# Performance work log

Measured on AMD Instinct MI355X. Metric: run time of the kernel, lower is better.

The kernel has to match this reference:

```python
import jax, jax.numpy as jnp
import numpy as np

B, S, HID = 1, 2048, 2048
NH, NKV = 32, 8
HD = HID // NH  # 64
WINDOW = 1024
ROPE_BASE = 500000.0


def setup_inputs() -> dict:
    key = jax.random.key(0)
    ks = jax.random.split(key, 5)
    sc = 0.02
    return {
        "hidden_states": jax.random.normal(ks[0], (B, S, HID), dtype=jnp.float32),
        "Wq": jax.random.normal(ks[1], (HID, NH * HD), dtype=jnp.float32) * sc,
        "Wk": jax.random.normal(ks[2], (HID, NKV * HD), dtype=jnp.float32) * sc,
        "Wv": jax.random.normal(ks[3], (HID, NKV * HD), dtype=jnp.float32) * sc,
        "Wo": jax.random.normal(ks[4], (NH * HD, HID), dtype=jnp.float32) * sc,
    }


def _rope_cos_sin(seq_len, dtype):
    inv_freq = 1.0 / (ROPE_BASE ** (jnp.arange(0, HD, 2, dtype=jnp.float32) / HD))
    pos = jnp.arange(seq_len, dtype=jnp.float32)
    freqs = pos[:, None] * inv_freq[None, :]          # [S, HD/2]
    emb = jnp.concatenate([freqs, freqs], axis=-1)    # [S, HD]
    return jnp.cos(emb).astype(dtype), jnp.sin(emb).astype(dtype)


def _rotate_half(x):
    x1, x2 = x[..., : HD // 2], x[..., HD // 2:]
    return jnp.concatenate([-x2, x1], axis=-1)


def reference(hidden_states, Wq, Wk, Wv, Wo):
    b, s, _ = hidden_states.shape
    q = (hidden_states @ Wq).reshape(b, s, NH, HD).transpose(0, 2, 1, 3)   # [B,NH,S,D]
    k = (hidden_states @ Wk).reshape(b, s, NKV, HD).transpose(0, 2, 1, 3)  # [B,NKV,S,D]
    v = (hidden_states @ Wv).reshape(b, s, NKV, HD).transpose(0, 2, 1, 3)

    cos, sin = _rope_cos_sin(s, hidden_states.dtype)  # [S, D]
    cos, sin = cos[None, None], sin[None, None]       # [1,1,S,D]
    q = q * cos + _rotate_half(q) * sin
    k = k * cos + _rotate_half(k) * sin

    n_rep = NH // NKV
    k = jnp.repeat(k, n_rep, axis=1)  # [B,NH,S,D]
    v = jnp.repeat(v, n_rep, axis=1)

    # sliding-window causal additive mask
    row = jnp.arange(s)[:, None]
    col = jnp.arange(s)[None, :]
    banned = (col > row) | (col < row - WINDOW + 1)
    mask = jnp.where(banned, jnp.float32(-jnp.inf), 0.0).astype(hidden_states.dtype)

    scale = 1.0 / np.sqrt(HD)
    scores = jnp.einsum("bhqd,bhkd->bhqk", q, k) * scale + mask
    attn = jax.nn.softmax(scores, axis=-1)
    out = jnp.einsum("bhqk,bhkd->bhqd", attn, v)          # [B,NH,S,D]
    out = out.transpose(0, 2, 1, 3).reshape(b, s, NH * HD)
    return out @ Wo
```

## Files before the change

kernel.cpp:

```cpp
#include <hip/hip_runtime.h>
#include <hip/hip_bf16.h>
#include <math.h>

#define S_LEN 2048
#define HID 2048
#define NH 32
#define NKV 8
#define HD 64
#define WINDOW 1024
#define QBLK 128
#define QKVN 3072

typedef __attribute__((ext_vector_type(8))) short bx8;
typedef __attribute__((ext_vector_type(4))) float fx4;
typedef __attribute__((ext_vector_type(8))) unsigned short us8;

#define GL_LDS16(gp, lp) \
    __builtin_amdgcn_global_load_lds((__attribute__((address_space(1))) const void*)(gp), \
                                     (__attribute__((address_space(3))) void*)(lp), 16, 0, 0)

__global__ __launch_bounds__(256) void prep_kernel(const float* __restrict__ hs,
                                                   const float* __restrict__ Wq,
                                                   const float* __restrict__ Wk,
                                                   const float* __restrict__ Wv,
                                                   const float* __restrict__ Wo,
                                                   float* __restrict__ cosT, float* __restrict__ sinT,
                                                   __hip_bfloat16* __restrict__ hsb,
                                                   __hip_bfloat16* __restrict__ WqkvT,
                                                   __hip_bfloat16* __restrict__ WoT) {
    __shared__ float tile[32][33];
    int b = blockIdx.x, t = threadIdx.x;
    if (b < 256) {
        int idx = b * 256 + t;
        int s = idx >> 5, f = idx & 31;
        double inv = exp(-2.0 * (double)f / 64.0 * log(500000.0));
        double ang = (double)s * inv;
        cosT[idx] = (float)cos(ang);
        sinT[idx] = (float)sin(ang);
        return;
    }
    b -= 256;
    if (b < 2048) {
        int i = (b * 256 + t) * 8;
        float4 a = *reinterpret_cast<const float4*>(&hs[i]);
        float4 c = *reinterpret_cast<const float4*>(&hs[i + 4]);
        __hip_bfloat16 o[8] __attribute__((aligned(16)));
        o[0] = __float2bfloat16(a.x); o[1] = __float2bfloat16(a.y);
        o[2] = __float2bfloat16(a.z); o[3] = __float2bfloat16(a.w);
        o[4] = __float2bfloat16(c.x); o[5] = __float2bfloat16(c.y);
        o[6] = __float2bfloat16(c.z); o[7] = __float2bfloat16(c.w);
        *reinterpret_cast<bx8*>(&hsb[i]) = *reinterpret_cast<bx8*>(o);
        return;
    }
    b -= 2048;
    const float* src; __hip_bfloat16* dst; int Nd, bx, by;
    if (b < 4096)      { src = Wq; dst = WqkvT;                        Nd = 2048; bx = b & 63; by = b >> 6; }
    else if (b < 5120) { b -= 4096; src = Wk; dst = WqkvT + (size_t)2048 * 2048; Nd = 512; bx = b & 15; by = b >> 4; }
    else if (b < 6144) { b -= 5120; src = Wv; dst = WqkvT + (size_t)2560 * 2048; Nd = 512; bx = b & 15; by = b >> 4; }
    else               { b -= 6144; src = Wo; dst = WoT;               Nd = 2048; bx = b & 63; by = b >> 6; }
    int n0 = bx * 32, k0 = by * 32, tx = t & 31, ty = t >> 5;
#pragma unroll
    for (int i = 0; i < 4; i++)
        tile[ty + 8 * i][tx] = src[(size_t)(k0 + ty + 8 * i) * Nd + n0 + tx];
    __syncthreads();
#pragma unroll
    for (int i = 0; i < 4; i++)
        dst[(size_t)(n0 + ty + 8 * i) * 2048 + k0 + tx] = __float2bfloat16(tile[tx][ty + 8 * i]);
}

__global__ __launch_bounds__(256) void ropev_kernel(__hip_bfloat16* __restrict__ QKV,
                                                    __hip_bfloat16* __restrict__ Vt,
                                                    const float* __restrict__ cosT,
                                                    const float* __restrict__ sinT) {
    __shared__ __hip_bfloat16 tile[32][33];
    int b = blockIdx.x, t = threadIdx.x;
    if (b < 10240) {
        int idx = b * 256 + t;
        int f = idx & 31;
        int head = (idx >> 5) % (NH + NKV);
        int s = idx / ((NH + NKV) * 32);
        float c  = cosT[(s << 5) + f];
        float sn = sinT[(s << 5) + f];
        __hip_bfloat16* p = (head < NH) ? (QKV + (size_t)s * QKVN + head * HD)
                                        : (QKV + (size_t)s * QKVN + 2048 + (head - NH) * HD);
        float x1 = __bfloat162float(p[f]), x2 = __bfloat162float(p[f + 32]);
        p[f]      = __float2bfloat16(x1 * c - x2 * sn);
        p[f + 32] = __float2bfloat16(x2 * c + x1 * sn);
        return;
    }
    b -= 10240;
    int s0 = (b & 63) * 32, d0 = (b >> 6) * 32;
    int tx = t & 31, ty = t >> 5;
#pragma unroll
    for (int i = 0; i < 4; i++)
        tile[ty + 8 * i][tx] = QKV[(size_t)(s0 + ty + 8 * i) * QKVN + 2560 + d0 + tx];
    __syncthreads();
#pragma unroll
    for (int i = 0; i < 4; i++)
        Vt[(size_t)(d0 + ty + 8 * i) * S_LEN + s0 + tx] = tile[tx][ty + 8 * i];
}

template <int OUTBF16>
__global__ __launch_bounds__(256) void gemm_pipe_kernel(const __hip_bfloat16* __restrict__ A,
                                                        const __hip_bfloat16* __restrict__ Bt,
                                                        void* __restrict__ Cp,
                                                        int M, int N, int K, int stripe) {
    __shared__ __hip_bfloat16 As[4][2048];
    __shared__ __hip_bfloat16 Bs[4][4096];

    const int bid = blockIdx.x;
    const int x = bid & 7, j = bid >> 3;
    const int bn = (x * stripe + j % stripe) * 128;
    const int bm = (j / stripe) * 64;

    const int t = threadIdx.x, w = t >> 6, l = t & 63;
    const int wr = (w >> 1) * 32, wc = (w & 1) * 64;
    const int lr = l & 15;
    const int rdslot = (((l >> 4) ^ ((lr >> 1) & 3))) * 8;
    const int srow = w * 16 + (l >> 2);
    const int scol = (((l & 3) ^ ((l >> 3) & 3))) * 8;
    const int ldsoff = w * 512;

    const __hip_bfloat16* ga0 = A + (size_t)(bm + srow) * K + scol;
    const __hip_bfloat16* gb0 = Bt + (size_t)(bn + srow) * K + scol;
    const size_t half = (size_t)64 * K;

    fx4 acc[2][4];
#pragma unroll
    for (int m = 0; m < 2; m++)
#pragma unroll
        for (int n = 0; n < 4; n++) acc[m][n] = (fx4){0.f, 0.f, 0.f, 0.f};

    const int T = K >> 5;

#define STAGE(kt, b)                                              \
    do {                                                          \
        const __hip_bfloat16* ga = ga0 + (kt) * 32;               \
        const __hip_bfloat16* gb = gb0 + (kt) * 32;               \
        GL_LDS16(ga,        &As[(b)][ldsoff]);                    \
        GL_LDS16(gb,        &Bs[(b)][ldsoff]);                    \
        GL_LDS16(gb + half, &Bs[(b)][2048 + ldsoff]);             \
    } while (0)

    STAGE(0, 0);
    STAGE(1, 1);
    STAGE(2, 2);

    for (int i = 0; i < T; i++) {
        const int r = i & 3;
        if (i + 2 < T)      asm volatile("s_waitcnt vmcnt(6)" ::: "memory");
        else if (i + 1 < T) asm volatile("s_waitcnt vmcnt(3)" ::: "memory");
        else                asm volatile("s_waitcnt vmcnt(0)" ::: "memory");
        __builtin_amdgcn_s_barrier();
        asm volatile("" ::: "memory");
        if (i + 3 < T) STAGE(i + 3, (i + 3) & 3);

        bx8 af[2], bf[4];
#pragma unroll
        for (int m = 0; m < 2; m++)
            af[m] = *reinterpret_cast<const bx8*>(&As[r][(wr + m * 16 + lr) * 32 + rdslot]);
#pragma unroll
        for (int n = 0; n < 4; n++)
            bf[n] = *reinterpret_cast<const bx8*>(&Bs[r][(wc + n * 16 + lr) * 32 + rdslot]);
#pragma unroll
        for (int m = 0; m < 2; m++)
#pragma unroll
            for (int n = 0; n < 4; n++)
                acc[m][n] = __builtin_amdgcn_mfma_f32_16x16x32_bf16(af[m], bf[n], acc[m][n], 0, 0, 0);
    }
#undef STAGE

    const int lq = (l >> 4) * 4;
#pragma unroll
    for (int m = 0; m < 2; m++)
#pragma unroll
        for (int n = 0; n < 4; n++)
#pragma unroll
            for (int r2 = 0; r2 < 4; r2++) {
                int row = bm + wr + m * 16 + lq + r2;
                int col = bn + wc + n * 16 + lr;
                float v = acc[m][n][r2];
                if (OUTBF16)
                    ((__hip_bfloat16*)Cp)[(size_t)row * N + col] = __float2bfloat16(v);
                else
                    ((float*)Cp)[(size_t)row * N + col] = v;
            }
}

__global__ __launch_bounds__(512, 4) void attn_kernel(const __hip_bfloat16* __restrict__ Q,
                                                      const __hip_bfloat16* __restrict__ Kg,
                                                      const __hip_bfloat16* __restrict__ Vtg,
                                                      __hip_bfloat16* __restrict__ Ab) {
    __shared__ __hip_bfloat16 Ks[2][4096];
    __shared__ __hip_bfloat16 Vs[2][4096];
    __shared__ __hip_bfloat16 Ps[QBLK * 64];

    const int bid = blockIdx.x;
    const int swz = (bid & 7) * 64 + (bid >> 3);
    const int h = swz >> 4, qi = swz & 15;
    const int qb = qi * QBLK;
    const int kvh = h >> 2;

    const int t = threadIdx.x, w = t >> 6, l = t & 63;
    const int lr = l & 15, g = l >> 4, lk = g * 8;
    const int qbw = qb + 16 * w;
    const int prow = 16 * w + lr;
    const int psz = (prow & 7) << 4;

    char* PsB = (char*)Ps;

    bx8 qa[2];
#pragma unroll
    for (int ks = 0; ks < 2; ks++)
        qa[ks] = *reinterpret_cast<const bx8*>(
            &Q[(size_t)(qbw + lr) * QKVN + h * HD + ks * 32 + lk]);

    fx4 ot[4];
#pragma unroll
    for (int n = 0; n < 4; n++) ot[n] = (fx4){0.f, 0.f, 0.f, 0.f};
    float mrow = -1e30f, srow = 0.f;

    const int k0_first = (qb >= 1024) ? (qb - 1024) : 0;
    const int k0_last  = qb + 64;
    const int wmax = qbw + 15;
    const int wlow = qbw - (WINDOW - 1);
    const int rowq = qbw + lr;

    const int sr = t >> 3, c8 = t & 7;
    const int scolsw = 8 * (c8 ^ (sr & 7));
    const int kcol = kvh * HD + scolsw;
    const int vrow = kvh * HD + sr;
    __hip_bfloat16* ldsK = &Ks[0][0] + (t >> 6) * 512;
    __hip_bfloat16* ldsV = &Vs[0][0] + (t >> 6) * 512;

#define ASTAGE(k0v, p)                                                           \
    do {                                                                         \
        GL_LDS16(&Kg[(size_t)((k0v) + sr) * QKVN + kcol], ldsK + (p) * 4096);    \
        GL_LDS16(&Vtg[(size_t)vrow * S_LEN + (k0v) + scolsw], ldsV + (p) * 4096);\
    } while (0)

    ASTAGE(k0_first, 0);

    int ti = 0;
    for (int k0 = k0_first; k0 <= k0_last; k0 += 64, ++ti) {
        const int p = ti & 1;
        asm volatile("s_waitcnt vmcnt(0)" ::: "memory");
        __builtin_amdgcn_s_barrier();
        asm volatile("" ::: "memory");
        if (k0 + 64 <= k0_last) ASTAGE(k0 + 64, p ^ 1);

        if (k0 <= wmax && k0 + 63 >= wlow) {
            char* KsB = (char*)&Ks[p][0];
            char* VsB = (char*)&Vs[p][0];
            bx8 kb[4][2];
#pragma unroll
            for (int n = 0; n < 4; n++)
#pragma unroll
                for (int ks = 0; ks < 2; ks++) {
                    int row = 16 * n + lr;
                    kb[n][ks] = *reinterpret_cast<const bx8*>(
                        KsB + row * 128 + (((ks * 64) + 16 * g) ^ ((row & 7) << 4)));
                }
            fx4 sc[4];
#pragma unroll
            for (int n = 0; n < 4; n++) {
                sc[n] = __builtin_amdgcn_mfma_f32_16x16x32_bf16(kb[n][0], qa[0],
                                                                (fx4){0.f, 0.f, 0.f, 0.f}, 0, 0, 0);
                sc[n] = __builtin_amdgcn_mfma_f32_16x16x32_bf16(kb[n][1], qa[1], sc[n], 0, 0, 0);
            }
            const bool interior = (k0 + 63 <= qbw) && (k0 >= qbw - 1008);
            if (interior) {
#pragma unroll
                for (int n = 0; n < 4; n++)
#pragma unroll
                    for (int r = 0; r < 4; r++) sc[n][r] *= 0.125f;
            } else {
#pragma unroll
                for (int n = 0; n < 4; n++)
#pragma unroll
                    for (int r = 0; r < 4; r++) {
                        int key = k0 + 16 * n + 4 * g + r;
                        bool valid = (key <= rowq) && (key >= rowq - (WINDOW - 1));
                        sc[n][r] = valid ? sc[n][r] * 0.125f : -1e30f;
                    }
            }
            float tmax = fmaxf(fmaxf(sc[0][0], sc[0][1]), fmaxf(sc[0][2], sc[0][3]));
#pragma unroll
            for (int n = 1; n < 4; n++)
                tmax = fmaxf(tmax, fmaxf(fmaxf(sc[n][0], sc[n][1]), fmaxf(sc[n][2], sc[n][3])));
            tmax = fmaxf(tmax, __shfl_xor(tmax, 16));
            tmax = fmaxf(tmax, __shfl_xor(tmax, 32));
            const bool grew = __any(tmax > mrow);
            float mn = mrow, fs = 1.f;
            if (grew) {
                mn = fmaxf(mrow, tmax);
                fs = __expf(mrow - mn);
                mrow = mn;
            }
            float ps = 0.f;
#pragma unroll
            for (int n = 0; n < 4; n++) {
#pragma unroll
                for (int r = 0; r < 4; r++) {
                    float p2 = __expf(sc[n][r] - mn);
                    sc[n][r] = p2;
                    ps += p2;
                }
                __hip_bfloat16 pk[4] __attribute__((aligned(8)));
                pk[0] = __float2bfloat16(sc[n][0]); pk[1] = __float2bfloat16(sc[n][1]);
                pk[2] = __float2bfloat16(sc[n][2]); pk[3] = __float2bfloat16(sc[n][3]);
                *reinterpret_cast<unsigned long long*>(PsB + prow * 128 + ((32 * n + 8 * g) ^ psz)) =
                    *reinterpret_cast<unsigned long long*>(pk);
            }
            ps += __shfl_xor(ps, 16);
            ps += __shfl_xor(ps, 32);
            if (grew) {
                srow = srow * fs + ps;
#pragma unroll
                for (int n = 0; n < 4; n++)
#pragma unroll
                    for (int r = 0; r < 4; r++) ot[n][r] *= fs;
            } else {
                srow += ps;
            }
            bx8 vb[4][2];
#pragma unroll
            for (int n = 0; n < 4; n++)
#pragma unroll
                for (int ks = 0; ks < 2; ks++) {
                    int row = 16 * n + lr;
                    vb[n][ks] = *reinterpret_cast<const bx8*>(
                        VsB + row * 128 + (((ks * 64) + 16 * g) ^ ((row & 7) << 4)));
                }
            bx8 pb[2];
#pragma unroll
            for (int ks = 0; ks < 2; ks++)
                pb[ks] = *reinterpret_cast<const bx8*>(
                    PsB + prow * 128 + (((ks * 64) + 16 * g) ^ psz));
#pragma unroll
            for (int n = 0; n < 4; n++) {
                ot[n] = __builtin_amdgcn_mfma_f32_16x16x32_bf16(vb[n][0], pb[0], ot[n], 0, 0, 0);
                ot[n] = __builtin_amdgcn_mfma_f32_16x16x32_bf16(vb[n][1], pb[1], ot[n], 0, 0, 0);
            }
        }
    }
#undef ASTAGE

    const float inv = 1.f / srow;
#pragma unroll
    for (int n = 0; n < 4; n++) {
        __hip_bfloat16 pk[4] __attribute__((aligned(8)));
#pragma unroll
        for (int r = 0; r < 4; r++) pk[r] = __float2bfloat16(ot[n][r] * inv);
        *reinterpret_cast<unsigned long long*>(PsB + prow * 128 + ((32 * n + 8 * g) ^ psz)) =
            *reinterpret_cast<unsigned long long*>(pk);
    }
    __syncthreads();
#pragma unroll
    for (int j = 0; j < 2; j++) {
        const int row = (t >> 3) + 64 * j, c = t & 7;
        us8 v = *reinterpret_cast<const us8*>(PsB + row * 128 + ((c * 16) ^ ((row & 7) << 4)));
        *reinterpret_cast<us8*>(&Ab[(size_t)(qb + row) * HID + h * HD + c * 8]) = v;
    }
}

extern "C" void kernel_launch(void* const* d_in, const int* in_sizes, int n_in,
                              void* d_out, int out_size, void* d_ws, size_t ws_size,
                              hipStream_t stream) {
    const float* hs = (const float*)d_in[0];
    const float* Wq = (const float*)d_in[1];
    const float* Wk = (const float*)d_in[2];
    const float* Wv = (const float*)d_in[3];
    const float* Wo = (const float*)d_in[4];

    float* ws   = (float*)d_ws;
    float* cosT = ws;
    float* sinT = cosT + 65536;
    __hip_bfloat16* hsb    = (__hip_bfloat16*)(sinT + 65536);
    __hip_bfloat16* WqkvT  = hsb + 4194304;
    __hip_bfloat16* WoT    = WqkvT + 6291456;
    __hip_bfloat16* QKVb   = WoT + 4194304;
    __hip_bfloat16* Vt     = QKVb + 6291456;
    __hip_bfloat16* Ab     = hsb;

    prep_kernel<<<12544, 256, 0, stream>>>(hs, Wq, Wk, Wv, Wo, cosT, sinT, hsb, WqkvT, WoT);

    gemm_pipe_kernel<1><<<768, 256, 0, stream>>>(hsb, WqkvT, QKVb, 2048, QKVN, 2048, 3);

    ropev_kernel<<<11264, 256, 0, stream>>>(QKVb, Vt, cosT, sinT);

    attn_kernel<<<512, 512, 0, stream>>>(QKVb, QKVb + 2048, Vt, Ab);

    gemm_pipe_kernel<0><<<512, 256, 0, stream>>>(Ab, WoT, d_out, 2048, 2048, 2048, 2);
}
```

Before: 144.2 us.

## Pre-pack GEMM operands into tile-contiguous swizzled layout for contiguous LDS loads

The prep kernel now writes hidden states and transposed weights in a tiled, pre-swizzled layout: each 64x32 (A) or 128x32 (B) k-tile is stored contiguously with the LDS XOR swizzle already applied. The GEMM kernel then streams each stage as one contiguous block indexed by thread id, instead of doing strided row loads with in-kernel swizzle addressing. This targets global-load coalescing in the GEMMs. The cost is more scattered 2-byte stores in the transpose part of prep, and the output-projection GEMM still reads the attention output unpacked.

```diff
diff --git a/kernel.cpp b/kernel.cpp
--- a/kernel.cpp
+++ b/kernel.cpp
@@ -18,6 +18,7 @@
 #define GL_LDS16(gp, lp) \
     __builtin_amdgcn_global_load_lds((__attribute__((address_space(1))) const void*)(gp), \
                                      (__attribute__((address_space(3))) void*)(lp), 16, 0, 0)
+
 
 __global__ __launch_bounds__(256) void prep_kernel(const float* __restrict__ hs,
                                                    const float* __restrict__ Wq,
@@ -42,6 +43,7 @@
     b -= 256;
     if (b < 2048) {
         int i = (b * 256 + t) * 8;
+        int m = i >> 11, k0 = i & 2047;
         float4 a = *reinterpret_cast<const float4*>(&hs[i]);
         float4 c = *reinterpret_cast<const float4*>(&hs[i + 4]);
         __hip_bfloat16 o[8] __attribute__((aligned(16)));
@@ -49,23 +51,32 @@
         o[2] = __float2bfloat16(a.z); o[3] = __float2bfloat16(a.w);
         o[4] = __float2bfloat16(c.x); o[5] = __float2bfloat16(c.y);
         o[6] = __float2bfloat16(c.z); o[7] = __float2bfloat16(c.w);
-        *reinterpret_cast<bx8*>(&hsb[i]) = *reinterpret_cast<bx8*>(o);
+        int mt = m >> 6, r = m & 63, kt = k0 >> 5;
+        int s2 = ((k0 & 31) >> 3) ^ ((r >> 1) & 3);
+        size_t dst = (size_t)(mt * 64 + kt) * 2048 + r * 32 + s2 * 8;
+        *reinterpret_cast<bx8*>(&hsb[dst]) = *reinterpret_cast<bx8*>(o);
         return;
     }
     b -= 2048;
-    const float* src; __hip_bfloat16* dst; int Nd, bx, by;
-    if (b < 4096)      { src = Wq; dst = WqkvT;                        Nd = 2048; bx = b & 63; by = b >> 6; }
-    else if (b < 5120) { b -= 4096; src = Wk; dst = WqkvT + (size_t)2048 * 2048; Nd = 512; bx = b & 15; by = b >> 4; }
-    else if (b < 6144) { b -= 5120; src = Wv; dst = WqkvT + (size_t)2560 * 2048; Nd = 512; bx = b & 15; by = b >> 4; }
-    else               { b -= 6144; src = Wo; dst = WoT;               Nd = 2048; bx = b & 63; by = b >> 6; }
+    const float* src; __hip_bfloat16* dst; int Nd, bx, by, gbase;
+    if (b < 4096)      { src = Wq; dst = WqkvT; Nd = 2048; bx = b & 63; by = b >> 6; gbase = 0; }
+    else if (b < 5120) { b -= 4096; src = Wk; dst = WqkvT; Nd = 512; bx = b & 15; by = b >> 4; gbase = 2048; }
+    else if (b < 6144) { b -= 5120; src = Wv; dst = WqkvT; Nd = 512; bx = b & 15; by = b >> 4; gbase = 2560; }
+    else               { b -= 6144; src = Wo; dst = WoT;   Nd = 2048; bx = b & 63; by = b >> 6; gbase = 0; }
     int n0 = bx * 32, k0 = by * 32, tx = t & 31, ty = t >> 5;
 #pragma unroll
     for (int i = 0; i < 4; i++)
         tile[ty + 8 * i][tx] = src[(size_t)(k0 + ty + 8 * i) * Nd + n0 + tx];
     __syncthreads();
-#pragma unroll
-    for (int i = 0; i < 4; i++)
-        dst[(size_t)(n0 + ty + 8 * i) * 2048 + k0 + tx] = __float2bfloat16(tile[tx][ty + 8 * i]);
+    const int kt = k0 >> 5, chunk = tx >> 3, ko = tx & 7;
+#pragma unroll
+    for (int i = 0; i < 4; i++) {
+        int gn = gbase + n0 + ty + 8 * i;
+        int nt = gn >> 7, r = gn & 127;
+        int s2 = chunk ^ ((r >> 1) & 3);
+        dst[(size_t)(nt * 64 + kt) * 4096 + r * 32 + s2 * 8 + ko] =
+            __float2bfloat16(tile[tx][ty + 8 * i]);
+    }
 }
 
 __global__ __launch_bounds__(256) void ropev_kernel(__hip_bfloat16* __restrict__ QKV,
@@ -100,9 +111,9 @@
         Vt[(size_t)(d0 + ty + 8 * i) * S_LEN + s0 + tx] = tile[tx][ty + 8 * i];
 }
 
-template <int OUTBF16>
+template <int APACKED, int OUTBF16>
 __global__ __launch_bounds__(256) void gemm_pipe_kernel(const __hip_bfloat16* __restrict__ A,
-                                                        const __hip_bfloat16* __restrict__ Bt,
+                                                        const __hip_bfloat16* __restrict__ Bpk,
                                                         void* __restrict__ Cp,
                                                         int M, int N, int K, int stripe) {
     __shared__ __hip_bfloat16 As[4][2048];
@@ -121,9 +132,10 @@
     const int scol = (((l & 3) ^ ((l >> 3) & 3))) * 8;
     const int ldsoff = w * 512;
 
-    const __hip_bfloat16* ga0 = A + (size_t)(bm + srow) * K + scol;
-    const __hip_bfloat16* gb0 = Bt + (size_t)(bn + srow) * K + scol;
-    const size_t half = (size_t)64 * K;
+    const __hip_bfloat16* ga0 = APACKED
+        ? A + (size_t)(bm >> 6) * 131072 + t * 8
+        : A + (size_t)(bm + srow) * K + scol;
+    const __hip_bfloat16* gb0 = Bpk + (size_t)(bn >> 7) * 262144 + t * 8;
 
     fx4 acc[2][4];
 #pragma unroll
@@ -133,13 +145,14 @@
 
     const int T = K >> 5;
 
-#define STAGE(kt, b)                                              \
-    do {                                                          \
-        const __hip_bfloat16* ga = ga0 + (kt) * 32;               \
-        const __hip_bfloat16* gb = gb0 + (kt) * 32;               \
-        GL_LDS16(ga,        &As[(b)][ldsoff]);                    \
-        GL_LDS16(gb,        &Bs[(b)][ldsoff]);                    \
-        GL_LDS16(gb + half, &Bs[(b)][2048 + ldsoff]);             \
+#define STAGE(kt, b)                                                      \
+    do {                                                                  \
+        const __hip_bfloat16* ga = APACKED ? ga0 + (kt) * 2048            \
+                                           : ga0 + (kt) * 32;             \
+        const __hip_bfloat16* gb = gb0 + (kt) * 4096;                     \
+        GL_LDS16(ga,        &As[(b)][ldsoff]);                            \
+        GL_LDS16(gb,        &Bs[(b)][ldsoff]);                            \
+        GL_LDS16(gb + 2048, &Bs[(b)][2048 + ldsoff]);                     \
     } while (0)
 
     STAGE(0, 0);
@@ -385,11 +398,11 @@
 
     prep_kernel<<<12544, 256, 0, stream>>>(hs, Wq, Wk, Wv, Wo, cosT, sinT, hsb, WqkvT, WoT);
 
-    gemm_pipe_kernel<1><<<768, 256, 0, stream>>>(hsb, WqkvT, QKVb, 2048, QKVN, 2048, 3);
+    gemm_pipe_kernel<1, 1><<<768, 256, 0, stream>>>(hsb, WqkvT, QKVb, 2048, QKVN, 2048, 3);
 
     ropev_kernel<<<11264, 256, 0, stream>>>(QKVb, Vt, cosT, sinT);
 
     attn_kernel<<<512, 512, 0, stream>>>(QKVb, QKVb + 2048, Vt, Ab);
 
-    gemm_pipe_kernel<0><<<512, 256, 0, stream>>>(Ab, WoT, d_out, 2048, 2048, 2048, 2);
+    gemm_pipe_kernel<0, 0><<<512, 256, 0, stream>>>(Ab, WoT, d_out, 2048, 2048, 2048, 2);
 }
```

Result: no change. 144.7 us (+0.3%).
